# Kernel optimization log

Measured on AMD Instinct MI355X. Metric: run time of the kernel, lower is better.

## Reference

```python
import jax, jax.numpy as jnp
import numpy as np
import math

R, C, B, E = 64, 256, 1, 768
H, DK, F = 8, 96, 3072
EPS = 1e-5


def _ln(x, w, b):
    m = jnp.mean(x, axis=-1, keepdims=True)
    v = jnp.var(x, axis=-1, keepdims=True)
    return (x - m) / jnp.sqrt(v + EPS) * w + b


def _lin(x, w, b):
    # torch Linear: y = x @ W^T + b, W: [out, in]
    return jnp.einsum('...i,oi->...o', x, w) + b


def setup_inputs() -> dict:
    key = jax.random.key(0)
    ks = jax.random.split(key, 16)
    w = lambda k, s: jax.random.normal(k, s, dtype=jnp.float32) * 0.02
    z = lambda s: jnp.zeros(s, dtype=jnp.float32)
    o = lambda s: jnp.ones(s, dtype=jnp.float32)
    return {
        'x': jax.random.normal(ks[0], (R, C, B, E), dtype=jnp.float32),
        'ln_row_w': o((E,)), 'ln_row_b': z((E,)),
        'row_q_w': w(ks[1], (E, E)), 'row_q_b': z((E,)),
        'row_k_w': w(ks[2], (E, E)), 'row_k_b': z((E,)),
        'row_v_w': w(ks[3], (E, E)), 'row_v_b': z((E,)),
        'row_o_w': w(ks[4], (E, E)), 'row_o_b': z((E,)),
        'ln_col_w': o((E,)), 'ln_col_b': z((E,)),
        'col_q_w': w(ks[5], (E, E)), 'col_q_b': z((E,)),
        'col_k_w': w(ks[6], (E, E)), 'col_k_b': z((E,)),
        'col_v_w': w(ks[7], (E, E)), 'col_v_b': z((E,)),
        'col_o_w': w(ks[8], (E, E)), 'col_o_b': z((E,)),
        'ln_ffn_w': o((E,)), 'ln_ffn_b': z((E,)),
        'fc1_w': w(ks[9], (F, E)), 'fc1_b': z((F,)),
        'fc2_w': w(ks[10], (E, F)), 'fc2_b': z((E,)),
    }


def reference(x, ln_row_w, ln_row_b, row_q_w, row_q_b, row_k_w, row_k_b,
              row_v_w, row_v_b, row_o_w, row_o_b,
              ln_col_w, ln_col_b, col_q_w, col_q_b, col_k_w, col_k_b,
              col_v_w, col_v_b, col_o_w, col_o_b,
              ln_ffn_w, ln_ffn_b, fc1_w, fc1_b, fc2_w, fc2_b):
    r, c, n, e = x.shape  # n_rows, n_cols, batch, embed

    # ---- Row self-attention (pre-LN residual block) ----
    xn = _ln(x, ln_row_w, ln_row_b)
    scaling = (DK ** -0.5) / math.sqrt(r)  # align_scaling: extra 1/sqrt(n_rows)
    q = _lin(xn, row_q_w, row_q_b).reshape(r, c, n, H, DK) * scaling
    k = _lin(xn, row_k_w, row_k_b).reshape(r, c, n, H, DK)
    v = _lin(xn, row_v_w, row_v_b).reshape(r, c, n, H, DK)
    row_logits = jnp.einsum('rinhd,rjnhd->hnij', q, k)  # sums over rows
    row_probs = jax.nn.softmax(row_logits, axis=-1)     # [H, B, C, C]
    rc = jnp.einsum('hnij,rjnhd->rinhd', row_probs, v).reshape(r, c, n, e)
    x = x + _lin(rc, row_o_w, row_o_b)

    # ---- Column self-attention (pre-LN residual block) ----
    xn = _ln(x, ln_col_w, ln_col_b)
    q = _lin(xn, col_q_w, col_q_b).reshape(r, c, n, H, DK) * (DK ** -0.5)
    k = _lin(xn, col_k_w, col_k_b).reshape(r, c, n, H, DK)
    v = _lin(xn, col_v_w, col_v_b).reshape(r, c, n, H, DK)
    col_logits = jnp.einsum('icnhd,jcnhd->hcnij', q, k)
    col_probs = jax.nn.softmax(col_logits, axis=-1)     # [H, C, B, R, R]
    cc = jnp.einsum('hcnij,jcnhd->icnhd', col_probs, v).reshape(r, c, n, e)
    x = x + _lin(cc, col_o_w, col_o_b)

    # ---- Feed-forward (pre-LN residual block) ----
    xn = _ln(x, ln_ffn_w, ln_ffn_b)
    h = jax.nn.gelu(_lin(xn, fc1_w, fc1_b), approximate=False)
    x = x + _lin(h, fc2_w, fc2_b)

    return x, row_probs, col_probs
```

## Files before the change

kernel.cpp:

```cpp
#include <hip/hip_runtime.h>
#include <cstdint>

typedef unsigned short u16;
typedef __attribute__((ext_vector_type(8))) short short8;
typedef __attribute__((ext_vector_type(4))) short short4v;
typedef __attribute__((ext_vector_type(4))) float floatx4;

#define DEV __device__ __forceinline__

DEV float bf2f(u16 u) { union { uint32_t i; float f; } w; w.i = ((uint32_t)u) << 16; return w.f; }
DEV u16 f2bf(float f) {
  union { float f; uint32_t i; } w; w.f = f;
  uint32_t x = w.i;
  return (u16)((x + 0x7fffu + ((x >> 16) & 1u)) >> 16);
}

DEV size_t poff(int row, int k, int nkt) {
  return ((size_t)((row >> 7) * nkt + (k >> 5))) * 4096 +
         (size_t)(((k >> 3) & 3) * 1024 + (row & 127) * 8 + (k & 7));
}

DEV float fast_gelu(float x) {
  const float y = x * 0.70710678118f;
  const float ay = fabsf(y);
  const float t = 1.f / (1.f + 0.3275911f * ay);
  const float poly = t * (0.254829592f + t * (-0.284496736f +
                     t * (1.421413741f + t * (-1.453152027f + t * 1.061405429f))));
  const float er = 1.f - poly * __expf(-y * y);
  const float erf_y = __builtin_copysignf(er, y);
  return 0.5f * x * (1.f + erf_y);
}

DEV void async_copy16(const u16* g, u16* l) {
  __builtin_amdgcn_global_load_lds(
      (const __attribute__((address_space(1))) void*)(uintptr_t)g,
      (__attribute__((address_space(3))) void*)(uint32_t)(uintptr_t)l,
      16, 0, 0);
}

struct CvtArgs {
  const float* src[10];
  float scale[10];
};
__global__ __launch_bounds__(256) void cvt_all(CvtArgs a, u16* __restrict__ dst) {
  const size_t e = ((size_t)blockIdx.x * 256 + threadIdx.x) * 4;
  if (e >= 9437184) return;
  int reg, N, K;
  size_t base;
  if (e < 4718592) { reg = (int)(e / 589824); base = (size_t)reg * 589824; N = 768; K = 768; }
  else if (e < 7077888) { reg = 8; base = 4718592; N = 3072; K = 768; }
  else { reg = 9; base = 7077888; N = 768; K = 3072; }
  const int NKT = K >> 5;
  const size_t r = e - base;
  const int tile = (int)(r >> 12);
  const int nt = tile / NKT, kt = tile - nt * NKT;
  const int rem = (int)(r & 4095);
  const int c = rem >> 10, row = (rem >> 3) & 127, j = rem & 7;
  const int n = nt * 128 + row, k = kt * 32 + c * 8 + j;
  const float sc = a.scale[reg];
  floatx4 f = *(const floatx4*)(a.src[reg] + (size_t)n * K + k);
  short4v o;
#pragma unroll
  for (int q = 0; q < 4; ++q) o[q] = (short)f2bf(f[q] * sc);
  *(short4v*)(dst + e) = o;
}

__global__ __launch_bounds__(256) void bias_pack(const float* __restrict__ qb,
                                                 const float* __restrict__ kb,
                                                 const float* __restrict__ vb,
                                                 float sq, float* __restrict__ out) {
  const int i = blockIdx.x * 256 + threadIdx.x;
  if (i >= 2304) return;
  const int buf = i / 768, c = i - buf * 768;
  out[i] = buf == 0 ? qb[c] * sq : (buf == 1 ? kb[c] : vb[c]);
}

template<bool INF32>
__global__ __launch_bounds__(256) void ln_kernel(const void* __restrict__ in,
                                                 const float* __restrict__ w,
                                                 const float* __restrict__ b,
                                                 u16* __restrict__ out) {
  const int wid = threadIdx.x >> 6, lane = threadIdx.x & 63;
  const int row = blockIdx.x * 4 + wid;
  const size_t base = (size_t)row * 768;
  float v[12];
#pragma unroll
  for (int p = 0; p < 3; ++p) {
    const int e = p * 256 + lane * 4;
    if constexpr (INF32) {
      floatx4 f = *(const floatx4*)((const float*)in + base + e);
#pragma unroll
      for (int j = 0; j < 4; ++j) v[p * 4 + j] = f[j];
    } else {
      short4v u = *(const short4v*)((const u16*)in + base + e);
#pragma unroll
      for (int j = 0; j < 4; ++j) v[p * 4 + j] = bf2f((u16)u[j]);
    }
  }
  float s = 0.f, sq = 0.f;
#pragma unroll
  for (int i = 0; i < 12; ++i) { s += v[i]; sq += v[i] * v[i]; }
#pragma unroll
  for (int m = 1; m < 64; m <<= 1) { s += __shfl_xor(s, m); sq += __shfl_xor(sq, m); }
  const float mean = s * (1.f / 768.f);
  const float var = sq * (1.f / 768.f) - mean * mean;
  const float rstd = rsqrtf(var + 1e-5f);
#pragma unroll
  for (int p = 0; p < 3; ++p) {
    const int e = p * 256 + lane * 4;
    floatx4 wv = *(const floatx4*)(w + e);
    floatx4 bv = *(const floatx4*)(b + e);
    short4v o;
#pragma unroll
    for (int j = 0; j < 4; ++j) {
      float y = (v[p * 4 + j] - mean) * rstd * wv[j] + bv[j];
      o[j] = (short)f2bf(y);
    }
    *(short4v*)(out + poff(row, e, 24)) = o;
  }
}

template<int AMODE, int AP, int BP>
DEV void stage_tile(const u16* __restrict__ Asrc, const u16* __restrict__ Bsrc,
                    int m0, int n0, int lda, int ldb, int kk0, int ktAbs, int t,
                    u16* ldsA, u16* ldsB) {
  const int wid = t >> 6, lane = t & 63;
  const int col = (((t & 3) ^ ((t >> 2) & 3)) << 3);
#pragma unroll
  for (int i = 0; i < 2; ++i) {
    const int slot = i * 4 + wid;
    const int r = i * 64 + (t >> 2);
    const int kk = kk0 + col;
    if constexpr (AP) {
      async_copy16(Asrc + (size_t)ktAbs * 4096 + slot * 512 + lane * 8, ldsA + slot * 512);
    } else {
      const u16* ga;
      if constexpr (AMODE == 0) {
        ga = Asrc + (size_t)(m0 + r) * lda + kk;
      } else {
        const int r96 = kk / 96, d = kk - r96 * 96;
        ga = Asrc + (size_t)r96 * 196608 + (size_t)(m0 + r) * 768 + d;
      }
      async_copy16(ga, ldsA + i * 2048 + wid * 512);
    }
    if constexpr (BP) {
      async_copy16(Bsrc + (size_t)ktAbs * 4096 + slot * 512 + lane * 8, ldsB + slot * 512);
    } else {
      const u16* gb;
      if constexpr (AMODE == 0) {
        gb = Bsrc + (size_t)(n0 + r) * ldb + kk;
      } else {
        const int r96 = kk / 96, d = kk - r96 * 96;
        gb = Bsrc + (size_t)r96 * 196608 + (size_t)(n0 + r) * 768 + d;
      }
      async_copy16(gb, ldsB + i * 2048 + wid * 512);
    }
  }
}

template<int AMODE, int EPI, int AP, int BP>
__global__ __launch_bounds__(256) void gemm_bt(
    const u16* __restrict__ A, const u16* __restrict__ B,
    const float* __restrict__ bias, const void* __restrict__ res,
    void* __restrict__ out, int K, int lda, int ldb,
    long long aBatch, long long bBatch, long long outBatch, int ldc, int bkt0,
    float scale) {
  __shared__ u16 lds[3 * 8192];
  const int t = threadIdx.x;
  const int z = blockIdx.z;
  const int m0 = blockIdx.x * 128, n0 = blockIdx.y * 128;
  const u16* Ab;
  const u16* Bb;
  int koff = 0;
  if constexpr (AMODE == 0) { Ab = A + (size_t)z * aBatch; Bb = B + (size_t)z * bBatch; }
  else { const int h = z >> 4; Ab = A + h * 96; Bb = B + h * 96; koff = (z & 15) * 384; }

  const u16* Astage;
  const u16* Bstage;
  if constexpr (AP) Astage = Ab + ((size_t)((m0 >> 7) * lda)) * 4096;
  else Astage = Ab;
  if constexpr (BP) Bstage = Bb + ((size_t)((n0 >> 7) * ldb + bkt0)) * 4096;
  else Bstage = Bb;

  const int wid = t >> 6, lane = t & 63;
  const int wr = wid >> 1, wc = wid & 1;
  const int lrow = lane & 15, lhi = lane >> 4;
  const int swl = lrow & 3;

  floatx4 acc[4][4];
#pragma unroll
  for (int i = 0; i < 4; ++i)
#pragma unroll
    for (int j = 0; j < 4; ++j) acc[i][j] = (floatx4){0.f, 0.f, 0.f, 0.f};

  const int NT = K >> 5;

  stage_tile<AMODE, AP, BP>(Astage, Bstage, m0, n0, lda, ldb, koff, 0, t, lds, lds + 4096);
  if (NT > 1)
    stage_tile<AMODE, AP, BP>(Astage, Bstage, m0, n0, lda, ldb, koff + 32, 1, t,
                              lds + 8192, lds + 8192 + 4096);
  if (NT > 2) asm volatile("s_waitcnt vmcnt(4)" ::: "memory");
  else        asm volatile("s_waitcnt vmcnt(0)" ::: "memory");
  __builtin_amdgcn_s_barrier();
  asm volatile("" ::: "memory");

  int cur = 0, nxt = 2;
  for (int kt = 0; kt < NT; ++kt) {
    const bool more = (kt + 2) < NT;
    if (more)
      stage_tile<AMODE, AP, BP>(Astage, Bstage, m0, n0, lda, ldb, koff + (kt + 2) * 32,
                                kt + 2, t, lds + nxt * 8192, lds + nxt * 8192 + 4096);

    const u16* lA = lds + cur * 8192;
    const u16* lB = lA + 4096;
    short8 af[4], bfr[4];
#pragma unroll
    for (int mi = 0; mi < 4; ++mi) {
      if constexpr (AP)
        af[mi] = *(const short8*)&lA[lhi * 1024 + (wr * 64 + mi * 16 + lrow) * 8];
      else
        af[mi] = *(const short8*)&lA[(wr * 64 + mi * 16 + lrow) * 32 + ((lhi ^ swl) << 3)];
    }
#pragma unroll
    for (int ni = 0; ni < 4; ++ni) {
      if constexpr (BP)
        bfr[ni] = *(const short8*)&lB[lhi * 1024 + (wc * 64 + ni * 16 + lrow) * 8];
      else
        bfr[ni] = *(const short8*)&lB[(wc * 64 + ni * 16 + lrow) * 32 + ((lhi ^ swl) << 3)];
    }

    __builtin_amdgcn_s_setprio(1);
#pragma unroll
    for (int mi = 0; mi < 4; ++mi)
#pragma unroll
      for (int ni = 0; ni < 4; ++ni)
        acc[mi][ni] = __builtin_amdgcn_mfma_f32_16x16x32_bf16(af[mi], bfr[ni], acc[mi][ni], 0, 0, 0);
    __builtin_amdgcn_s_setprio(0);

    if (kt + 1 < NT) {
      if (more) asm volatile("s_waitcnt vmcnt(4)" ::: "memory");
      else      asm volatile("s_waitcnt vmcnt(0)" ::: "memory");
      __builtin_amdgcn_s_barrier();
      asm volatile("" ::: "memory");
    }
    cur = (cur == 2) ? 0 : cur + 1;
    nxt = (nxt == 2) ? 0 : nxt + 1;
  }

  const int mbase = m0 + wr * 64;
  const int nbase = n0 + wc * 64;
#pragma unroll
  for (int mi = 0; mi < 4; ++mi) {
#pragma unroll
    for (int ni = 0; ni < 4; ++ni) {
      const int n = nbase + ni * 16 + lrow;
      float bz = 0.f;
      if constexpr (EPI != 1 && EPI != 7) { if (bias) bz = bias[n]; }
#pragma unroll
      for (int r4 = 0; r4 < 4; ++r4) {
        const int m = mbase + mi * 16 + lhi * 4 + r4;
        const float val = acc[mi][ni][r4];
        if constexpr (EPI == 1) {
          ((float*)out)[(size_t)z * outBatch + (size_t)m * ldc + n] = val;
        } else if constexpr (EPI == 2) {
          ((u16*)out)[poff(m, n, ldc >> 5)] = f2bf(fast_gelu(val + bz));
        } else if constexpr (EPI == 3) {
          const float r = ((const float*)res)[(size_t)m * ldc + n];
          ((float*)out)[(size_t)m * ldc + n] = r + val + bz;
        } else if constexpr (EPI == 4) {
          const float r = ((const float*)res)[(size_t)m * ldc + n];
          ((u16*)out)[(size_t)m * ldc + n] = f2bf(r + val + bz);
        } else if constexpr (EPI == 7) {
          const int rr = n / 96, d = n - rr * 96;
          ((u16*)out)[poff(rr * 256 + m, z * 96 + d, 24)] = f2bf(val);
        } else if constexpr (EPI == 8) {
          const int buf = n / 768, col = n - buf * 768;
          ((u16*)out)[(size_t)buf * 12582912 + (size_t)m * 768 + col] = f2bf(val + bz);
        }
      }
    }
  }
}

__global__ __launch_bounds__(256) void softmax_row(const float* __restrict__ part,
                                                   float* __restrict__ probs_f,
                                                   u16* __restrict__ probs_b) {
  const int wid = threadIdx.x >> 6, lane = threadIdx.x & 63;
  const int row = blockIdx.x * 4 + wid;
  const int h = row >> 8, i = row & 255;
  const size_t base = (size_t)h * 16 * 65536 + (size_t)i * 256 + lane * 4;
  floatx4 v = (floatx4){0.f, 0.f, 0.f, 0.f};
#pragma unroll
  for (int s16 = 0; s16 < 16; ++s16) {
    floatx4 p = *(const floatx4*)(part + base + (size_t)s16 * 65536);
#pragma unroll
    for (int j = 0; j < 4; ++j) v[j] += p[j];
  }
  float mx = fmaxf(fmaxf(v[0], v[1]), fmaxf(v[2], v[3]));
#pragma unroll
  for (int m = 1; m < 64; m <<= 1) mx = fmaxf(mx, __shfl_xor(mx, m));
  float e[4], s = 0.f;
#pragma unroll
  for (int j = 0; j < 4; ++j) { e[j] = __expf(v[j] - mx); s += e[j]; }
#pragma unroll
  for (int m = 1; m < 64; m <<= 1) s += __shfl_xor(s, m);
  const float inv = 1.f / s;
  floatx4 of;
  short4v ob;
#pragma unroll
  for (int j = 0; j < 4; ++j) {
    const float p = e[j] * inv;
    of[j] = p;
    ob[j] = (short)f2bf(p);
  }
  *(floatx4*)(probs_f + (size_t)row * 256 + lane * 4) = of;
  *(short4v*)(probs_b + (size_t)h * 65536 + poff(i, lane * 4, 8)) = ob;
}

__global__ __launch_bounds__(256) void pack_vt(const u16* __restrict__ v, u16* __restrict__ vt) {
  __shared__ u16 S[64][104];
  const int jb = blockIdx.x, r = blockIdx.y, h = blockIdx.z;
  const int t = threadIdx.x;
#pragma unroll
  for (int p = 0; p < 3; ++p) {
    const int cid = t + p * 256;
    const int j = cid / 12, ch = cid - j * 12;
    short8 x = *(const short8*)&v[((size_t)(r * 256 + jb * 64 + j)) * 768 + h * 96 + ch * 8];
    *(short8*)&S[j][ch * 8] = x;
  }
  __syncthreads();
#pragma unroll
  for (int p = 0; p < 3; ++p) {
    const int cid = t + p * 256;
    const int d = cid / 8, cj = cid - d * 8;
    u16 tmp[8];
#pragma unroll
    for (int m = 0; m < 8; ++m) tmp[m] = S[cj * 8 + m][d];
    const int row_t = r * 96 + d;
    const int k = jb * 64 + cj * 8;
    *(short8*)&vt[(size_t)h * 1572864 + poff(row_t, k, 8)] = *(short8*)tmp;
  }
}

__global__ __launch_bounds__(256) void col_attn(const u16* __restrict__ q,
                                                const u16* __restrict__ k,
                                                const u16* __restrict__ v,
                                                float* __restrict__ probs,
                                                u16* __restrict__ ctx) {
  __shared__ u16 qs[64][104];
  __shared__ u16 ks[64][104];
  __shared__ u16 vt[96][72];
  __shared__ u16 ps[64][72];
  const int c = blockIdx.x, h = blockIdx.y;
  const int t = threadIdx.x;
#pragma unroll
  for (int p = 0; p < 3; ++p) {
    const int cid = t + p * 256;
    const int i = cid / 12, ch = cid - i * 12;
    const size_t g = ((size_t)(i * 256 + c)) * 768 + h * 96 + ch * 8;
    short8 qv = *(const short8*)(q + g);
    short8 kv = *(const short8*)(k + g);
    short8 vv = *(const short8*)(v + g);
    *(short8*)&qs[i][ch * 8] = qv;
    *(short8*)&ks[i][ch * 8] = kv;
#pragma unroll
    for (int m = 0; m < 8; ++m) vt[ch * 8 + m][i] = (u16)vv[m];
  }
  __syncthreads();
  const int lane = t & 63, wid = t >> 6;
  const int lrow = lane & 15, lhi = lane >> 4;

  floatx4 s[4];
#pragma unroll
  for (int nj = 0; nj < 4; ++nj) s[nj] = (floatx4){0.f, 0.f, 0.f, 0.f};
#pragma unroll
  for (int kk = 0; kk < 3; ++kk) {
    short8 a = *(const short8*)&qs[wid * 16 + lrow][kk * 32 + lhi * 8];
#pragma unroll
    for (int nj = 0; nj < 4; ++nj) {
      short8 bb = *(const short8*)&ks[nj * 16 + lrow][kk * 32 + lhi * 8];
      s[nj] = __builtin_amdgcn_mfma_f32_16x16x32_bf16(a, bb, s[nj], 0, 0, 0);
    }
  }
  const size_t pb = ((size_t)(h * 256 + c)) * 4096;
#pragma unroll
  for (int r4 = 0; r4 < 4; ++r4) {
    float mx = fmaxf(fmaxf(s[0][r4], s[1][r4]), fmaxf(s[2][r4], s[3][r4]));
    mx = fmaxf(mx, __shfl_xor(mx, 1));
    mx = fmaxf(mx, __shfl_xor(mx, 2));
    mx = fmaxf(mx, __shfl_xor(mx, 4));
    mx = fmaxf(mx, __shfl_xor(mx, 8));
    float e[4], sum = 0.f;
#pragma unroll
    for (int nj = 0; nj < 4; ++nj) { e[nj] = __expf(s[nj][r4] - mx); sum += e[nj]; }
    sum += __shfl_xor(sum, 1);
    sum += __shfl_xor(sum, 2);
    sum += __shfl_xor(sum, 4);
    sum += __shfl_xor(sum, 8);
    const float inv = 1.f / sum;
    const int i = wid * 16 + lhi * 4 + r4;
#pragma unroll
    for (int nj = 0; nj < 4; ++nj) {
      const float pv = e[nj] * inv;
      const int j = nj * 16 + lrow;
      probs[pb + (size_t)i * 64 + j] = pv;
      ps[i][j] = f2bf(pv);
    }
  }
  __syncthreads();
  floatx4 o[6];
#pragma unroll
  for (int df = 0; df < 6; ++df) o[df] = (floatx4){0.f, 0.f, 0.f, 0.f};
#pragma unroll
  for (int k2 = 0; k2 < 2; ++k2) {
    short8 a = *(const short8*)&ps[wid * 16 + lrow][k2 * 32 + lhi * 8];
#pragma unroll
    for (int df = 0; df < 6; ++df) {
      short8 bb = *(const short8*)&vt[df * 16 + lrow][k2 * 32 + lhi * 8];
      o[df] = __builtin_amdgcn_mfma_f32_16x16x32_bf16(a, bb, o[df], 0, 0, 0);
    }
  }
#pragma unroll
  for (int df = 0; df < 6; ++df)
#pragma unroll
    for (int r4 = 0; r4 < 4; ++r4) {
      const int i = wid * 16 + lhi * 4 + r4;
      const int d = df * 16 + lrow;
      ctx[poff(i * 256 + c, h * 96 + d, 24)] = f2bf(o[df][r4]);
    }
}

extern "C" void kernel_launch(void* const* d_in, const int* in_sizes, int n_in,
                              void* d_out, int out_size, void* d_ws, size_t ws_size,
                              hipStream_t stream) {
  const float* x_in  = (const float*)d_in[0];
  const float* lnr_w = (const float*)d_in[1];
  const float* lnr_b = (const float*)d_in[2];
  const float* rq_w  = (const float*)d_in[3];
  const float* rq_b  = (const float*)d_in[4];
  const float* rk_w  = (const float*)d_in[5];
  const float* rk_b  = (const float*)d_in[6];
  const float* rv_w  = (const float*)d_in[7];
  const float* rv_b  = (const float*)d_in[8];
  const float* ro_w  = (const float*)d_in[9];
  const float* ro_b  = (const float*)d_in[10];
  const float* lnc_w = (const float*)d_in[11];
  const float* lnc_b = (const float*)d_in[12];
  const float* cq_w  = (const float*)d_in[13];
  const float* cq_b  = (const float*)d_in[14];
  const float* ck_w  = (const float*)d_in[15];
  const float* ck_b  = (const float*)d_in[16];
  const float* cv_w  = (const float*)d_in[17];
  const float* cv_b  = (const float*)d_in[18];
  const float* co_w  = (const float*)d_in[19];
  const float* co_b  = (const float*)d_in[20];
  const float* lnf_w = (const float*)d_in[21];
  const float* lnf_b = (const float*)d_in[22];
  const float* f1_w  = (const float*)d_in[23];
  const float* f1_b  = (const float*)d_in[24];
  const float* f2_w  = (const float*)d_in[25];
  const float* f2_b  = (const float*)d_in[26];

  const float s_row = 0.0127577591f;
  const float s_col = 0.1020620726f;

  char* ws = (char*)d_ws;
  const size_t WSZ_E = 589824 * 2;
  u16* w_all = (u16*)ws;
  u16* w_rqkv = w_all;
  u16* w_ro   = (u16*)(ws + 3 * WSZ_E);
  u16* w_cqkv = (u16*)(ws + 4 * WSZ_E);
  u16* w_co   = (u16*)(ws + 7 * WSZ_E);
  u16* w_f1   = (u16*)(ws + 8 * WSZ_E);
  u16* w_f2   = (u16*)(ws + 8 * WSZ_E + 4718592);
  size_t off = 8 * WSZ_E + 2 * 4718592;

  const bool xf32 = ws_size >= 147849216ULL;
  char* x_cur = ws + off;
  off += xf32 ? 50331648 : 25165824;
  u16* qb = (u16*)(ws + off); off += 25165824;
  u16* kb = (u16*)(ws + off); off += 25165824;
  u16* vb = (u16*)(ws + off); off += 25165824;
  u16* probsb = (u16*)(ws + off); off += 1048576;
  float* qkvb_row = (float*)(ws + off); off += 9216;
  float* qkvb_col = (float*)(ws + off); off += 9216;

  u16* vt     = qb;
  u16* ctx1   = kb;
  u16* hidden = qb;
  u16* xn3    = vb;

  float* out_x  = (float*)d_out;
  float* out_rp = out_x + 12582912;
  float* out_cp = out_x + 13107200;
  u16* xn   = (u16*)out_x;
  u16* ctx2 = (u16*)((char*)out_x + 25165824);
  float* part = out_x;

  const dim3 blk(256);

  CvtArgs ca;
  ca.src[0] = rq_w; ca.src[1] = rk_w; ca.src[2] = rv_w; ca.src[3] = ro_w;
  ca.src[4] = cq_w; ca.src[5] = ck_w; ca.src[6] = cv_w; ca.src[7] = co_w;
  ca.src[8] = f1_w; ca.src[9] = f2_w;
  for (int i = 0; i < 10; ++i) ca.scale[i] = 1.f;
  ca.scale[0] = s_row; ca.scale[4] = s_col;
  cvt_all<<<9216, blk, 0, stream>>>(ca, w_all);
  bias_pack<<<9, blk, 0, stream>>>(rq_b, rk_b, rv_b, s_row, qkvb_row);
  bias_pack<<<9, blk, 0, stream>>>(cq_b, ck_b, cv_b, s_col, qkvb_col);

  ln_kernel<true><<<4096, blk, 0, stream>>>(x_in, lnr_w, lnr_b, xn);
  gemm_bt<0, 8, 1, 1><<<dim3(128, 18, 1), blk, 0, stream>>>(xn, w_rqkv, qkvb_row, nullptr, qb, 768, 24, 24, 0, 0, 0, 768, 0, 1.f);
  gemm_bt<2, 1, 0, 0><<<dim3(2, 2, 128), blk, 0, stream>>>(qb, kb, nullptr, nullptr, part, 384, 0, 0, 0, 0, 65536LL, 256, 0, 1.f);
  softmax_row<<<512, blk, 0, stream>>>(part, out_rp, probsb);
  pack_vt<<<dim3(4, 64, 8), blk, 0, stream>>>(vb, vt);
  gemm_bt<0, 7, 1, 1><<<dim3(2, 48, 8), blk, 0, stream>>>(probsb, vt, nullptr, nullptr, ctx1, 256, 8, 8, 65536LL, 1572864LL, 0, 0, 0, 1.f);
  if (xf32)
    gemm_bt<0, 3, 1, 1><<<dim3(128, 6, 1), blk, 0, stream>>>(ctx1, w_ro, ro_b, x_in, x_cur, 768, 24, 24, 0, 0, 0, 768, 0, 1.f);
  else
    gemm_bt<0, 4, 1, 1><<<dim3(128, 6, 1), blk, 0, stream>>>(ctx1, w_ro, ro_b, x_in, x_cur, 768, 24, 24, 0, 0, 0, 768, 0, 1.f);

  if (xf32) ln_kernel<true><<<4096, blk, 0, stream>>>(x_cur, lnc_w, lnc_b, xn);
  else      ln_kernel<false><<<4096, blk, 0, stream>>>(x_cur, lnc_w, lnc_b, xn);
  gemm_bt<0, 8, 1, 1><<<dim3(128, 18, 1), blk, 0, stream>>>(xn, w_cqkv, qkvb_col, nullptr, qb, 768, 24, 24, 0, 0, 0, 768, 0, 1.f);
  col_attn<<<dim3(256, 8), blk, 0, stream>>>(qb, kb, vb, out_cp, ctx2);
  if (xf32)
    gemm_bt<0, 3, 1, 1><<<dim3(128, 6, 1), blk, 0, stream>>>(ctx2, w_co, co_b, x_cur, x_cur, 768, 24, 24, 0, 0, 0, 768, 0, 1.f);
  else
    gemm_bt<0, 4, 1, 1><<<dim3(128, 6, 1), blk, 0, stream>>>(ctx2, w_co, co_b, x_cur, x_cur, 768, 24, 24, 0, 0, 0, 768, 0, 1.f);

  if (xf32) ln_kernel<true><<<4096, blk, 0, stream>>>(x_cur, lnf_w, lnf_b, xn3);
  else      ln_kernel<false><<<4096, blk, 0, stream>>>(x_cur, lnf_w, lnf_b, xn3);
  gemm_bt<0, 2, 1, 1><<<dim3(128, 12, 1), blk, 0, stream>>>(xn3, w_f1, f1_b, nullptr, hidden, 768, 24, 24, 0, 0, 0, 1536, 0, 1.f);
  gemm_bt<0, 3, 1, 1><<<dim3(128, 6, 1), blk, 0, stream>>>(hidden, w_f2, f2_b, x_cur, out_x, 1536, 48, 96, 0, 0, 0, 768, 0, 1.f);
  gemm_bt<0, 2, 1, 1><<<dim3(128, 12, 1), blk, 0, stream>>>(xn3, w_f1 + 1536 * 768, f1_b + 1536, nullptr, hidden, 768, 24, 24, 0, 0, 0, 1536, 0, 1.f);
  gemm_bt<0, 3, 1, 1><<<dim3(128, 6, 1), blk, 0, stream>>>(hidden, w_f2, nullptr, out_x, out_x, 1536, 48, 96, 0, 0, 0, 768, 48, 1.f);
}
```

Before: 624.2 us.

## Add 256x256-tile 512-thread GEMM with 4-stage async pipeline for QKV and FC1

Adds a new gemm_big kernel that computes 256x256 output tiles with 8 waves. Each wave holds a 128x64 accumulator block, and a 4-buffer async-copy LDS pipeline overlaps loads with MFMA work. The kernel replaces the 128-tile gemm_bt launches for the row and column QKV projections and both FC1 halves. The aim is more data reuse per loaded tile and better latency hiding. The cost is heavy register pressure from 32 accumulators per thread, 128KB of LDS per block, and fewer blocks per launch.

Result: slower. 682.1 us (+9.3%).

```diff
diff --git a/kernel.cpp b/kernel.cpp
--- a/kernel.cpp
+++ b/kernel.cpp
@@ -117,6 +117,101 @@
       o[j] = (short)f2bf(y);
     }
     *(short4v*)(out + poff(row, e, 24)) = o;
+  }
+}
+
+template<int EPI>
+__global__ __launch_bounds__(512) void gemm_big(
+    const u16* __restrict__ A, const u16* __restrict__ B,
+    const float* __restrict__ bias, void* __restrict__ out,
+    int K, int ldaT, int ldbT, int ldc, int bkt0) {
+  __shared__ u16 lds[4 * 16384];
+  const int t = threadIdx.x;
+  const int m0 = blockIdx.x * 256, n0 = blockIdx.y * 256;
+  const u16* Ab = A + ((size_t)((m0 >> 7) * ldaT)) * 4096;
+  const u16* Bb = B + ((size_t)((n0 >> 7) * ldbT + bkt0)) * 4096;
+  const int wid = t >> 6, lane = t & 63;
+  const int wr = wid >> 2, wc = wid & 3;
+  const int lrow = lane & 15, lhi = lane >> 4;
+
+  floatx4 acc[8][4];
+#pragma unroll
+  for (int i = 0; i < 8; ++i)
+#pragma unroll
+    for (int j = 0; j < 4; ++j) acc[i][j] = (floatx4){0.f, 0.f, 0.f, 0.f};
+
+  const int NT = K >> 5;
+
+#define STAGE(kt, buf)                                                        \
+  {                                                                           \
+    const int _kt = (kt);                                                     \
+    u16* const db = (u16*)lds + (buf) * 16384 + wid * 512;                    \
+    async_copy16(Ab + ((size_t)_kt) * 4096 + wid * 512 + lane * 8, db);       \
+    async_copy16(Ab + ((size_t)(ldaT + _kt)) * 4096 + wid * 512 + lane * 8, db + 4096); \
+    async_copy16(Bb + ((size_t)_kt) * 4096 + wid * 512 + lane * 8, db + 8192); \
+    async_copy16(Bb + ((size_t)(ldbT + _kt)) * 4096 + wid * 512 + lane * 8, db + 12288); \
+  }
+
+  STAGE(0, 0);
+  if (NT > 1) STAGE(1, 1);
+  if (NT > 2) STAGE(2, 2);
+  if (NT > 2)      asm volatile("s_waitcnt vmcnt(8)" ::: "memory");
+  else if (NT > 1) asm volatile("s_waitcnt vmcnt(4)" ::: "memory");
+  else             asm volatile("s_waitcnt vmcnt(0)" ::: "memory");
+  __builtin_amdgcn_s_barrier();
+  asm volatile("" ::: "memory");
+
+  for (int kt = 0; kt < NT; ++kt) {
+    if (kt + 3 < NT) STAGE(kt + 3, (kt + 3) & 3);
+
+    const u16* lA = lds + (kt & 3) * 16384 + wr * 4096;
+    const u16* lB = lds + (kt & 3) * 16384 + 8192 + (wc >> 1) * 4096;
+    short8 af[8], bfr[4];
+#pragma unroll
+    for (int mi = 0; mi < 8; ++mi)
+      af[mi] = *(const short8*)&lA[lhi * 1024 + (mi * 16 + lrow) * 8];
+#pragma unroll
+    for (int ni = 0; ni < 4; ++ni)
+      bfr[ni] = *(const short8*)&lB[lhi * 1024 + ((wc & 1) * 64 + ni * 16 + lrow) * 8];
+
+    __builtin_amdgcn_s_setprio(1);
+#pragma unroll
+    for (int mi = 0; mi < 8; ++mi)
+#pragma unroll
+      for (int ni = 0; ni < 4; ++ni)
+        acc[mi][ni] = __builtin_amdgcn_mfma_f32_16x16x32_bf16(af[mi], bfr[ni], acc[mi][ni], 0, 0, 0);
+    __builtin_amdgcn_s_setprio(0);
+
+    if (kt + 1 < NT) {
+      if (kt + 3 < NT)      asm volatile("s_waitcnt vmcnt(8)" ::: "memory");
+      else if (kt + 2 < NT) asm volatile("s_waitcnt vmcnt(4)" ::: "memory");
+      else                  asm volatile("s_waitcnt vmcnt(0)" ::: "memory");
+      __builtin_amdgcn_s_barrier();
+      asm volatile("" ::: "memory");
+    }
+  }
+#undef STAGE
+
+  const int mbase = m0 + wr * 128;
+  const int nbase = n0 + wc * 64;
+#pragma unroll
+  for (int mi = 0; mi < 8; ++mi) {
+#pragma unroll
+    for (int ni = 0; ni < 4; ++ni) {
+      const int n = nbase + ni * 16 + lrow;
+      const float bz = bias ? bias[n] : 0.f;
+#pragma unroll
+      for (int r4 = 0; r4 < 4; ++r4) {
+        const int m = mbase + mi * 16 + lhi * 4 + r4;
+        const float val = acc[mi][ni][r4];
+        if constexpr (EPI == 2) {
+          ((u16*)out)[poff(m, n, ldc >> 5)] = f2bf(fast_gelu(val + bz));
+        } else {
+          const int buf = n / 768, col = n - buf * 768;
+          ((u16*)out)[(size_t)buf * 12582912 + (size_t)m * 768 + col] = f2bf(val + bz);
+        }
+      }
+    }
   }
 }
 
@@ -498,6 +593,7 @@
   float* part = out_x;
 
   const dim3 blk(256);
+  const dim3 blk512(512);
 
   CvtArgs ca;
   ca.src[0] = rq_w; ca.src[1] = rk_w; ca.src[2] = rv_w; ca.src[3] = ro_w;
@@ -510,7 +606,7 @@
   bias_pack<<<9, blk, 0, stream>>>(cq_b, ck_b, cv_b, s_col, qkvb_col);
 
   ln_kernel<true><<<4096, blk, 0, stream>>>(x_in, lnr_w, lnr_b, xn);
-  gemm_bt<0, 8, 1, 1><<<dim3(128, 18, 1), blk, 0, stream>>>(xn, w_rqkv, qkvb_row, nullptr, qb, 768, 24, 24, 0, 0, 0, 768, 0, 1.f);
+  gemm_big<8><<<dim3(64, 9), blk512, 0, stream>>>(xn, w_rqkv, qkvb_row, qb, 768, 24, 24, 768, 0);
   gemm_bt<2, 1, 0, 0><<<dim3(2, 2, 128), blk, 0, stream>>>(qb, kb, nullptr, nullptr, part, 384, 0, 0, 0, 0, 65536LL, 256, 0, 1.f);
   softmax_row<<<512, blk, 0, stream>>>(part, out_rp, probsb);
   pack_vt<<<dim3(4, 64, 8), blk, 0, stream>>>(vb, vt);
@@ -522,7 +618,7 @@
 
   if (xf32) ln_kernel<true><<<4096, blk, 0, stream>>>(x_cur, lnc_w, lnc_b, xn);
   else      ln_kernel<false><<<4096, blk, 0, stream>>>(x_cur, lnc_w, lnc_b, xn);
-  gemm_bt<0, 8, 1, 1><<<dim3(128, 18, 1), blk, 0, stream>>>(xn, w_cqkv, qkvb_col, nullptr, qb, 768, 24, 24, 0, 0, 0, 768, 0, 1.f);
+  gemm_big<8><<<dim3(64, 9), blk512, 0, stream>>>(xn, w_cqkv, qkvb_col, qb, 768, 24, 24, 768, 0);
   col_attn<<<dim3(256, 8), blk, 0, stream>>>(qb, kb, vb, out_cp, ctx2);
   if (xf32)
     gemm_bt<0, 3, 1, 1><<<dim3(128, 6, 1), blk, 0, stream>>>(ctx2, w_co, co_b, x_cur, x_cur, 768, 24, 24, 0, 0, 0, 768, 0, 1.f);
@@ -531,8 +627,8 @@
 
   if (xf32) ln_kernel<true><<<4096, blk, 0, stream>>>(x_cur, lnf_w, lnf_b, xn3);
   else      ln_kernel<false><<<4096, blk, 0, stream>>>(x_cur, lnf_w, lnf_b, xn3);
-  gemm_bt<0, 2, 1, 1><<<dim3(128, 12, 1), blk, 0, stream>>>(xn3, w_f1, f1_b, nullptr, hidden, 768, 24, 24, 0, 0, 0, 1536, 0, 1.f);
+  gemm_big<2><<<dim3(64, 6), blk512, 0, stream>>>(xn3, w_f1, f1_b, hidden, 768, 24, 24, 1536, 0);
   gemm_bt<0, 3, 1, 1><<<dim3(128, 6, 1), blk, 0, stream>>>(hidden, w_f2, f2_b, x_cur, out_x, 1536, 48, 96, 0, 0, 0, 768, 0, 1.f);
-  gemm_bt<0, 2, 1, 1><<<dim3(128, 12, 1), blk, 0, stream>>>(xn3, w_f1 + 1536 * 768, f1_b + 1536, nullptr, hidden, 768, 24, 24, 0, 0, 0, 1536, 0, 1.f);
+  gemm_big<2><<<dim3(64, 6), blk512, 0, stream>>>(xn3, w_f1 + 1536 * 768, f1_b + 1536, hidden, 768, 24, 24, 1536, 0);
   gemm_bt<0, 3, 1, 1><<<dim3(128, 6, 1), blk, 0, stream>>>(hidden, w_f2, nullptr, out_x, out_x, 1536, 48, 96, 0, 0, 0, 768, 48, 1.f);
 }
```
